# Kernel optimization log

Hardware: AMD Instinct MI355X
Metric: run time of the kernel (lower is better)

Reference implementation:

```python
import jax, jax.numpy as jnp
import numpy as np

B, N, H = 512, 128, 256      # graphs, nodes per graph, hidden
NH, HD = 8, 32               # heads, head dim
DEG = 8
E = B * N * DEG              # 524288 edges
BN_EPS = 1e-5


def setup_inputs() -> dict:
    key = jax.random.key(0)
    ks = jax.random.split(key, 16)

    def w(k, shape):
        return jax.random.normal(k, shape, dtype=jnp.float32) * 0.02

    # intra-graph random edges: base offset per graph, local src/dst in [0, N)
    base = jnp.repeat(jnp.arange(B, dtype=jnp.int32) * N, N * DEG)
    edge_src = base + jax.random.randint(ks[1], (E,), 0, N, dtype=jnp.int32)
    edge_dst = base + jax.random.randint(ks[2], (E,), 0, N, dtype=jnp.int32)

    return {
        "h": jax.random.normal(ks[0], (B * N, H), dtype=jnp.float32),
        "edge_src": edge_src,
        "edge_dst": edge_dst,
        "gin_w1": w(ks[3], (H, H)), "gin_b1": jnp.zeros((H,), jnp.float32),
        "gin_w2": w(ks[4], (H, H)), "gin_b2": jnp.zeros((H,), jnp.float32),
        "attn_in_w": w(ks[5], (3 * H, H)), "attn_in_b": jnp.zeros((3 * H,), jnp.float32),
        "attn_out_w": w(ks[6], (H, H)), "attn_out_b": jnp.zeros((H,), jnp.float32),
        "bn_local_g": jnp.ones((H,), jnp.float32), "bn_local_b": jnp.zeros((H,), jnp.float32),
        "bn_attn_g": jnp.ones((H,), jnp.float32), "bn_attn_b": jnp.zeros((H,), jnp.float32),
        "bn_out_g": jnp.ones((H,), jnp.float32), "bn_out_b": jnp.zeros((H,), jnp.float32),
        "ffn1_w": w(ks[7], (2 * H, H)), "ffn1_b": jnp.zeros((2 * H,), jnp.float32),
        "ffn2_w": w(ks[8], (H, 2 * H)), "ffn2_b": jnp.zeros((H,), jnp.float32),
    }


def _bn(x, g, b):
    # nn.BatchNorm1d training-mode forward: batch stats over node dim, biased var
    mean = jnp.mean(x, axis=0)
    var = jnp.mean(jnp.square(x - mean), axis=0)
    return g * (x - mean) * jax.lax.rsqrt(var + BN_EPS) + b


def _mha(x, in_w, in_b, out_w, out_b):
    # x: [B, N, H]; uniform graphs -> key_padding_mask is all-valid
    qkv = x @ in_w.T + in_b                           # [B, N, 3H]
    q, k, v = jnp.split(qkv, 3, axis=-1)
    def heads(t):
        return t.reshape(B, N, NH, HD).transpose(0, 2, 1, 3)  # [B, NH, N, HD]
    q, k, v = heads(q), heads(k), heads(v)
    scores = jnp.einsum('bhqd,bhkd->bhqk', q, k) / jnp.sqrt(jnp.float32(HD))
    att = jax.nn.softmax(scores, axis=-1)
    o = jnp.einsum('bhqk,bhkd->bhqd', att, v).transpose(0, 2, 1, 3).reshape(B, N, H)
    return o @ out_w.T + out_b


def reference(h, edge_src, edge_dst,
              gin_w1, gin_b1, gin_w2, gin_b2,
              attn_in_w, attn_in_b, attn_out_w, attn_out_b,
              bn_local_g, bn_local_b, bn_attn_g, bn_attn_b, bn_out_g, bn_out_b,
              ffn1_w, ffn1_b, ffn2_w, ffn2_b):
    # --- local GIN branch: (1+eps)*h + sum_{j in N(i)} h_j, eps=0, then 2-layer MLP
    agg = jax.ops.segment_sum(h[edge_src], edge_dst, num_segments=B * N)
    z = h + agg
    h_local = jax.nn.relu(z @ gin_w1.T + gin_b1) @ gin_w2.T + gin_b2
    h_local = _bn(h + h_local, bn_local_g, bn_local_b)

    # --- global attention branch (to_dense_batch is an exact reshape here)
    h_dense = h.reshape(B, N, H)
    h_attn = _mha(h_dense, attn_in_w, attn_in_b, attn_out_w, attn_out_b).reshape(B * N, H)
    h_attn = _bn(h + h_attn, bn_attn_g, bn_attn_b)

    # --- combine + FFN + out norm
    x = h_local + h_attn
    x = x + jax.nn.relu(x @ ffn1_w.T + ffn1_b) @ ffn2_w.T + ffn2_b
    return _bn(x, bn_out_g, bn_out_b)
```

## Files before the change

kernel.cpp:

```cpp
#include <hip/hip_runtime.h>
#include <hip/hip_bf16.h>

#define B_   512
#define N_   128
#define H_   256
#define NH_  8
#define HD_  32
#define DEG_ 8
#define R_   (B_ * N_)
#define E_   (B_ * N_ * DEG_)
#define EPG_ (N_ * DEG_)

typedef unsigned short u16;
typedef unsigned int u32;

typedef __attribute__((ext_vector_type(8))) short s16x8;
typedef __attribute__((ext_vector_type(4))) float f32x4;

__device__ __forceinline__ float b2f(u16 u) {
  union { u32 i; float f; } v;
  v.i = ((u32)u) << 16;
  return v.f;
}
__device__ __forceinline__ u16 f2b(float f) {
  union { float f; u32 u; } v;
  v.f = f;
  u32 r = (v.u + 0x7fffu + ((v.u >> 16) & 1u)) >> 16;
  return (u16)r;
}
__device__ __forceinline__ void ld4b(const u16* p, float* o) {
  ushort4 v = *(const ushort4*)p;
  o[0] = b2f(v.x); o[1] = b2f(v.y); o[2] = b2f(v.z); o[3] = b2f(v.w);
}

__device__ __forceinline__ int tix(int row, int col) {
  return ((row >> 7) << 15) + (((col >> 6) & 3) << 13) + ((row & 127) << 6) +
         (((((col >> 3) & 7) ^ (row & 7))) << 3) + (col & 7);
}


#define OFF_GW1 0
#define OFF_GB1 65536
#define OFF_GW2 65792
#define OFF_GB2 131328
#define OFF_AIW 131584
#define OFF_AIB 328192
#define OFF_AOW 328960
#define OFF_AOB 394496
#define OFF_F1W 394752
#define OFF_F1B 525824
#define OFF_F2W 526336
#define OFF_F2B 657408
#define W_TOTAL 657664

__global__ void zero_stats(float* __restrict__ st) {
  st[blockIdx.x * 256 + threadIdx.x] = 0.f;
}

__global__ __launch_bounds__(256) void cvt_h(const float* __restrict__ src,
                                             u16* __restrict__ dst) {
  const int e = (blockIdx.x * 256 + threadIdx.x) * 4;
  const float4 v = *(const float4*)(src + e);
  ushort4 o;
  o.x = f2b(v.x); o.y = f2b(v.y); o.z = f2b(v.z); o.w = f2b(v.w);
  *(ushort4*)(dst + tix(e >> 8, e & 255)) = o;
}

__global__ __launch_bounds__(256) void cvt_w(
    const float* s0, const float* s1, const float* s2, const float* s3,
    const float* s4, const float* s5, const float* s6, const float* s7,
    const float* s8, const float* s9, const float* s10, const float* s11,
    u16* __restrict__ dst) {
  const int sizes[12] = {65536, 256, 65536, 256, 196608, 768,
                         65536, 256, 131072, 512, 131072, 256};
  const float* srcs[12] = {s0, s1, s2, s3, s4, s5, s6, s7, s8, s9, s10, s11};
  int gid = (blockIdx.x * 256 + threadIdx.x) * 4;
  if (gid >= W_TOTAL) return;
  int seg = 0, off = gid;
  while (off >= sizes[seg]) { off -= sizes[seg]; seg++; }
  const float4 v = *(const float4*)(srcs[seg] + off);
  ushort4 o;
  o.x = f2b(v.x); o.y = f2b(v.y); o.z = f2b(v.z); o.w = f2b(v.w);
  *(ushort4*)(dst + gid) = o;
}

#define SROWS_ 32

__global__ __launch_bounds__(256) void agg_kernel(
    const u16* __restrict__ h, const int* __restrict__ esrc,
    const int* __restrict__ edst, u16* __restrict__ z) {
  __shared__ int s_src[EPG_];
  __shared__ int s_cnt[SROWS_];
  __shared__ int s_off[SROWS_ + 1];
  __shared__ int s_pos[SROWS_];
  const int g = blockIdx.x;
  const int r0 = blockIdx.y * SROWS_;
  const int t = threadIdx.x;

  if (t < SROWS_) s_cnt[t] = 0;
  __syncthreads();

  const int ebase = g * EPG_;
  int dl[4], sg[4];
#pragma unroll
  for (int i = 0; i < 4; i++) {
    const int e = ebase + t + i * 256;
    sg[i] = esrc[e];
    dl[i] = edst[e] - g * N_ - r0;
    if ((unsigned)dl[i] < SROWS_) atomicAdd(&s_cnt[dl[i]], 1);
  }
  __syncthreads();
  if (t == 0) {
    int acc = 0;
#pragma unroll
    for (int i = 0; i < SROWS_; i++) { s_off[i] = acc; acc += s_cnt[i]; }
    s_off[SROWS_] = acc;
  }
  __syncthreads();
  if (t < SROWS_) s_pos[t] = s_off[t];
  __syncthreads();
#pragma unroll
  for (int i = 0; i < 4; i++) {
    if ((unsigned)dl[i] < SROWS_) {
      const int slot = atomicAdd(&s_pos[dl[i]], 1);
      s_src[slot] = sg[i];
    }
  }
  __syncthreads();

  const int rg = t >> 5;
  const int c0 = (t & 31) * 8;
  for (int ib = 0; ib < SROWS_; ib += 8) {
    const int i = ib + rg;
    const int row = g * N_ + r0 + i;
    float acc[8];
    {
      const s16x8 v = *(const s16x8*)(h + tix(row, c0));
#pragma unroll
      for (int j = 0; j < 8; j++) acc[j] = b2f((u16)v[j]);
    }
    const int e0 = s_off[i], e1 = s_off[i + 1];
    for (int e = e0; e < e1; e++) {
      const int src = s_src[e];
      const s16x8 v = *(const s16x8*)(h + tix(src, c0));
#pragma unroll
      for (int j = 0; j < 8; j++) acc[j] += b2f((u16)v[j]);
    }
    s16x8 o;
#pragma unroll
    for (int j = 0; j < 8; j++) o[j] = (short)f2b(acc[j]);
    *(s16x8*)(z + tix(row, c0)) = o;
  }
}

template <int NC, int K, int RELU, int RES, int STATS, int ASPLIT, int CMODE>
__global__ __launch_bounds__(256) void gemm_mfma(
    const u16* A, const u16* A2,
    const u16* __restrict__ W, const u16* __restrict__ bias,
    const u16* res, u16* C0, u16* C1, u16* C2,
    float* __restrict__ gsum, float* __restrict__ gsq) {
  __shared__ u16 As[2][128 * 64] __attribute__((aligned(16)));
  __shared__ u16 Bs[2][128 * 64] __attribute__((aligned(16)));

  const int t = threadIdx.x;
  const int wave = t >> 6, lane = t & 63;
  const int wr = wave >> 1, wc = wave & 1;
  const int quad = lane >> 4, ln15 = lane & 15;
  const int row0 = blockIdx.x * 128, col0 = blockIdx.y * 128;

  f32x4 acc[4][4];
#pragma unroll
  for (int i = 0; i < 4; i++)
#pragma unroll
    for (int j = 0; j < 4; j++) acc[i][j] = (f32x4){0.f, 0.f, 0.f, 0.f};

  auto stage = [&](int b, int kt) {
    const u16* Ab;
    int ksl;
    if (ASPLIT) {
      if (kt < 256) { Ab = A; ksl = kt >> 6; } else { Ab = A2; ksl = (kt - 256) >> 6; }
    } else {
      Ab = A; ksl = kt >> 6;
    }
    const u16* abase = Ab + ((size_t)blockIdx.x << 15) + (ksl << 13);
#pragma unroll
    for (int i = 0; i < 4; i++) {
      const int fid = t + i * 256;
      __builtin_amdgcn_global_load_lds(
          (const __attribute__((address_space(1))) void*)(abase + fid * 8),
          (__attribute__((address_space(3))) void*)(&As[b][fid * 8]), 16, 0, 0);
      const int row = fid >> 3;
      const int segp = (fid & 7) ^ (row & 7);
      const u16* gw = W + (size_t)(col0 + row) * K + kt + segp * 8;
      __builtin_amdgcn_global_load_lds(
          (const __attribute__((address_space(1))) void*)gw,
          (__attribute__((address_space(3))) void*)(&Bs[b][fid * 8]), 16, 0, 0);
    }
  };

  stage(0, 0);
  for (int kt = 0; kt < K; kt += 64) {
    const int cur = (kt >> 6) & 1;
    if (kt + 64 < K) {
      stage(cur ^ 1, kt + 64);
      asm volatile("s_waitcnt vmcnt(8)" ::: "memory");
    } else {
      asm volatile("s_waitcnt vmcnt(0)" ::: "memory");
    }
    __builtin_amdgcn_s_barrier();
#pragma unroll
    for (int ks = 0; ks < 64; ks += 32) {
      s16x8 af[4], bf[4];
#pragma unroll
      for (int i = 0; i < 4; i++) {
        const int ra = wr * 64 + i * 16 + ln15;
        af[i] = *(const s16x8*)(
            &As[cur][ra * 64 + ((((ks >> 3) + quad) ^ (ra & 7)) * 8)]);
      }
#pragma unroll
      for (int j = 0; j < 4; j++) {
        const int rb = wc * 64 + j * 16 + ln15;
        bf[j] = *(const s16x8*)(
            &Bs[cur][rb * 64 + ((((ks >> 3) + quad) ^ (rb & 7)) * 8)]);
      }
#pragma unroll
      for (int i = 0; i < 4; i++)
#pragma unroll
        for (int j = 0; j < 4; j++)
          acc[i][j] = __builtin_amdgcn_mfma_f32_16x16x32_bf16(af[i], bf[j], acc[i][j], 0, 0, 0);
    }
    __builtin_amdgcn_s_barrier();
  }

  const int cbase = col0 + wc * 64;
  u16* Cb;
  int coff;
  if (CMODE) {
    const int chunk = col0 >> 8;
    Cb = (chunk == 0) ? C0 : ((chunk == 1) ? C1 : C2);
    coff = (col0 & 255) + wc * 64;
  } else {
    Cb = C0; coff = cbase;
  }

  float bs[4];
#pragma unroll
  for (int j = 0; j < 4; j++) bs[j] = b2f(bias[cbase + j * 16 + ln15]);

  float ssum[4] = {}, ssq[4] = {};
#pragma unroll
  for (int i = 0; i < 4; i++) {
    const int rbase = row0 + wr * 64 + i * 16 + quad * 4;
#pragma unroll
    for (int reg = 0; reg < 4; reg++) {
      const int row = rbase + reg;
#pragma unroll
      for (int j = 0; j < 4; j++) {
        float val = acc[i][j][reg] + bs[j];
        if (RELU) val = fmaxf(val, 0.f);
        if (RES) val += b2f(res[tix(row, cbase + j * 16 + ln15)]);
        Cb[tix(row, coff + j * 16 + ln15)] = f2b(val);
        if (STATS) { ssum[j] += val; ssq[j] += val * val; }
      }
    }
  }

  if (STATS) {
#pragma unroll
    for (int j = 0; j < 4; j++) {
      float s = ssum[j];
      s += __shfl_xor(s, 16);
      s += __shfl_xor(s, 32);
      float q = ssq[j];
      q += __shfl_xor(q, 16);
      q += __shfl_xor(q, 32);
      if (lane < 16) {
        atomicAdd(&gsum[cbase + j * 16 + lane], s);
        atomicAdd(&gsq[cbase + j * 16 + lane], q);
      }
    }
  }
}

__global__ __launch_bounds__(256) void attn_mfma(
    const u16* q, const u16* __restrict__ k,
    const u16* __restrict__ v, u16* o) {
  __shared__ u16 lds[21760] __attribute__((aligned(16)));
  u16* Vt = lds;
  u16* Qs = lds + 4352;
  u16* Ks = lds + 4352 + 5120;
  u16* P  = lds + 4352;

  const int g = blockIdx.x >> 3;
  const int hd = blockIdx.x & 7;
  const int t = threadIdx.x;
  const int wave = t >> 6, lane = t & 63;
  const int quad = lane >> 4, ln15 = lane & 15;
  const int strip = wave * 32;
  const float scale = 0.1767766952966369f;

#pragma unroll
  for (int i = 0; i < 4; i++) {
    const int fid = t + i * 256;
    const int row = fid >> 3;
    const int seg = fid & 7;
    const int gidx = tix(g * N_ + row, hd * HD_ + seg * 4);
    const ushort4 qv = *(const ushort4*)(q + gidx);
    const ushort4 kv = *(const ushort4*)(k + gidx);
    const ushort4 vv = *(const ushort4*)(v + gidx);
    ushort4 qs;
    qs.x = f2b(b2f(qv.x) * scale); qs.y = f2b(b2f(qv.y) * scale);
    qs.z = f2b(b2f(qv.z) * scale); qs.w = f2b(b2f(qv.w) * scale);
    *(ushort4*)(Qs + row * 40 + seg * 4) = qs;
    *(ushort4*)(Ks + row * 40 + seg * 4) = kv;
    Vt[(seg * 4 + 0) * 136 + row] = vv.x;
    Vt[(seg * 4 + 1) * 136 + row] = vv.y;
    Vt[(seg * 4 + 2) * 136 + row] = vv.z;
    Vt[(seg * 4 + 3) * 136 + row] = vv.w;
  }
  __syncthreads();

  s16x8 af[2], bf[8];
#pragma unroll
  for (int mi = 0; mi < 2; mi++)
    af[mi] = *(const s16x8*)(Qs + (strip + mi * 16 + ln15) * 40 + quad * 8);
#pragma unroll
  for (int nj = 0; nj < 8; nj++)
    bf[nj] = *(const s16x8*)(Ks + (nj * 16 + ln15) * 40 + quad * 8);

  f32x4 acc[2][8];
#pragma unroll
  for (int mi = 0; mi < 2; mi++)
#pragma unroll
    for (int nj = 0; nj < 8; nj++)
      acc[mi][nj] = __builtin_amdgcn_mfma_f32_16x16x32_bf16(
          af[mi], bf[nj], (f32x4){0.f, 0.f, 0.f, 0.f}, 0, 0, 0);

  __syncthreads();

#pragma unroll
  for (int mi = 0; mi < 2; mi++) {
#pragma unroll
    for (int reg = 0; reg < 4; reg++) {
      float mx = acc[mi][0][reg];
#pragma unroll
      for (int j = 1; j < 8; j++) mx = fmaxf(mx, acc[mi][j][reg]);
      mx = fmaxf(mx, __shfl_xor(mx, 1));
      mx = fmaxf(mx, __shfl_xor(mx, 2));
      mx = fmaxf(mx, __shfl_xor(mx, 4));
      mx = fmaxf(mx, __shfl_xor(mx, 8));
      float e[8], s = 0.f;
#pragma unroll
      for (int j = 0; j < 8; j++) { e[j] = __expf(acc[mi][j][reg] - mx); s += e[j]; }
      s += __shfl_xor(s, 1);
      s += __shfl_xor(s, 2);
      s += __shfl_xor(s, 4);
      s += __shfl_xor(s, 8);
      const float inv = 1.f / s;
      const int prow = strip + mi * 16 + quad * 4 + reg;
#pragma unroll
      for (int j = 0; j < 8; j++)
        P[prow * 136 + j * 16 + ln15] = f2b(e[j] * inv);
    }
  }
  __syncthreads();

  f32x4 acc2[2][2];
#pragma unroll
  for (int mi = 0; mi < 2; mi++)
#pragma unroll
    for (int nj = 0; nj < 2; nj++) acc2[mi][nj] = (f32x4){0.f, 0.f, 0.f, 0.f};
#pragma unroll
  for (int kt = 0; kt < 4; kt++) {
    s16x8 paf[2], vbf[2];
#pragma unroll
    for (int mi = 0; mi < 2; mi++)
      paf[mi] = *(const s16x8*)(P + (strip + mi * 16 + ln15) * 136 + kt * 32 + quad * 8);
#pragma unroll
    for (int nj = 0; nj < 2; nj++)
      vbf[nj] = *(const s16x8*)(Vt + (nj * 16 + ln15) * 136 + kt * 32 + quad * 8);
#pragma unroll
    for (int mi = 0; mi < 2; mi++)
#pragma unroll
      for (int nj = 0; nj < 2; nj++)
        acc2[mi][nj] = __builtin_amdgcn_mfma_f32_16x16x32_bf16(
            paf[mi], vbf[nj], acc2[mi][nj], 0, 0, 0);
  }

#pragma unroll
  for (int mi = 0; mi < 2; mi++)
#pragma unroll
    for (int nj = 0; nj < 2; nj++)
#pragma unroll
      for (int reg = 0; reg < 4; reg++) {
        const int row = strip + mi * 16 + quad * 4 + reg;
        o[tix(g * N_ + row, hd * HD_ + nj * 16 + ln15)] =
            f2b(acc2[mi][nj][reg]);
      }
}

__global__ void bn_finalize(const float* __restrict__ sum,
                            const float* __restrict__ sq,
                            const float* __restrict__ g,
                            const float* __restrict__ bb,
                            float* __restrict__ a, float* __restrict__ b) {
  const int c = threadIdx.x;
  const float mean = sum[c] * (1.f / R_);
  const float var = fmaxf(sq[c] * (1.f / R_) - mean * mean, 0.f);
  const float ai = g[c] * rsqrtf(var + 1e-5f);
  a[c] = ai;
  b[c] = bb[c] - mean * ai;
}

__global__ __launch_bounds__(256) void combine_kernel(
    const u16* __restrict__ rl, const u16* __restrict__ ra,
    const float* __restrict__ st, u16* __restrict__ x) {
  const int e = (blockIdx.x * 256 + threadIdx.x) * 4;
  const int col = e & 255;
  const int idx = tix(e >> 8, col);
  float rl4[4], ra4[4];
  ld4b(rl + idx, rl4);
  ld4b(ra + idx, ra4);
  const float* al = st + 1536;
  const float* bl = st + 1792;
  const float* aa = st + 2048;
  const float* ba = st + 2304;
  ushort4 o;
  u16* ov = (u16*)&o;
#pragma unroll
  for (int j = 0; j < 4; j++)
    ov[j] = f2b(al[col + j] * rl4[j] + bl[col + j] + aa[col + j] * ra4[j] + ba[col + j]);
  *(ushort4*)(x + idx) = o;
}

__global__ __launch_bounds__(256) void final_kernel(
    const u16* __restrict__ y, const float* __restrict__ st,
    float* __restrict__ out) {
  const int e = (blockIdx.x * 256 + threadIdx.x) * 4;
  const int col = e & 255;
  float y4[4];
  ld4b(y + tix(e >> 8, col), y4);
  const float* ao = st + 2560;
  const float* bo = st + 2816;
  float4 o;
  o.x = ao[col + 0] * y4[0] + bo[col + 0];
  o.y = ao[col + 1] * y4[1] + bo[col + 1];
  o.z = ao[col + 2] * y4[2] + bo[col + 2];
  o.w = ao[col + 3] * y4[3] + bo[col + 3];
  *(float4*)(out + e) = o;
}

extern "C" void kernel_launch(void* const* d_in, const int* in_sizes, int n_in,
                              void* d_out, int out_size, void* d_ws, size_t ws_size,
                              hipStream_t stream) {
  const float* h = (const float*)d_in[0];
  const int* esrc = (const int*)d_in[1];
  const int* edst = (const int*)d_in[2];
  const float* bn_local_g = (const float*)d_in[11];
  const float* bn_local_b = (const float*)d_in[12];
  const float* bn_attn_g = (const float*)d_in[13];
  const float* bn_attn_b = (const float*)d_in[14];
  const float* bn_out_g = (const float*)d_in[15];
  const float* bn_out_b = (const float*)d_in[16];

  const size_t RH = (size_t)R_ * H_;
  float* stats = (float*)d_ws;
  u16* WB = (u16*)((char*)d_ws + 65536);
  u16* Hb = (u16*)((char*)d_ws + 65536 + 2097152);
  u16* S1 = Hb + RH;
  u16* S2 = S1 + RH;
  u16* OD = (u16*)d_out;
  float* outf = (float*)d_out;

  zero_stats<<<12, 256, 0, stream>>>(stats);
  cvt_h<<<(int)(RH / 4 / 256), 256, 0, stream>>>(h, Hb);
  cvt_w<<<(W_TOTAL / 4 + 255) / 256, 256, 0, stream>>>(
      (const float*)d_in[3], (const float*)d_in[4], (const float*)d_in[5],
      (const float*)d_in[6], (const float*)d_in[7], (const float*)d_in[8],
      (const float*)d_in[9], (const float*)d_in[10], (const float*)d_in[17],
      (const float*)d_in[18], (const float*)d_in[19], (const float*)d_in[20], WB);

  gemm_mfma<768, 256, 0, 0, 0, 0, 1><<<dim3(512, 6), 256, 0, stream>>>(
      Hb, nullptr, WB + OFF_AIW, WB + OFF_AIB, nullptr, S1, S2, OD, nullptr, nullptr);
  attn_mfma<<<B_ * NH_, 256, 0, stream>>>(S1, S2, OD, S1);
  gemm_mfma<256, 256, 0, 1, 1, 0, 0><<<dim3(512, 2), 256, 0, stream>>>(
      S1, nullptr, WB + OFF_AOW, WB + OFF_AOB, Hb, S2, nullptr, nullptr,
      stats + 512, stats + 768);
  agg_kernel<<<dim3(B_, 4), 256, 0, stream>>>(Hb, esrc, edst, OD);
  gemm_mfma<256, 256, 1, 0, 0, 0, 0><<<dim3(512, 2), 256, 0, stream>>>(
      OD, nullptr, WB + OFF_GW1, WB + OFF_GB1, nullptr, S1, nullptr, nullptr,
      nullptr, nullptr);
  gemm_mfma<256, 256, 0, 1, 1, 0, 0><<<dim3(512, 2), 256, 0, stream>>>(
      S1, nullptr, WB + OFF_GW2, WB + OFF_GB2, Hb, OD, nullptr, nullptr,
      stats + 0, stats + 256);

  bn_finalize<<<1, 256, 0, stream>>>(stats + 0, stats + 256, bn_local_g,
                                     bn_local_b, stats + 1536, stats + 1792);
  bn_finalize<<<1, 256, 0, stream>>>(stats + 512, stats + 768, bn_attn_g,
                                     bn_attn_b, stats + 2048, stats + 2304);

  combine_kernel<<<(int)(RH / 4 / 256), 256, 0, stream>>>(OD, S2, stats, S1);
  gemm_mfma<512, 256, 1, 0, 0, 0, 1><<<dim3(512, 4), 256, 0, stream>>>(
      S1, nullptr, WB + OFF_F1W, WB + OFF_F1B, nullptr, S2, OD, nullptr,
      nullptr, nullptr);
  gemm_mfma<256, 512, 0, 1, 1, 1, 0><<<dim3(512, 2), 256, 0, stream>>>(
      S2, OD, WB + OFF_F2W, WB + OFF_F2B, S1, S1, nullptr, nullptr,
      stats + 1024, stats + 1280);

  bn_finalize<<<1, 256, 0, stream>>>(stats + 1024, stats + 1280, bn_out_g,
                                     bn_out_b, stats + 2560, stats + 2816);
  final_kernel<<<(int)(RH / 4 / 256), 256, 0, stream>>>(S1, stats, outf);
}
```

Measured before the change: 612.9 us.

## Fuse two-layer MLPs into one kernel keeping hidden activations in LDS

Adds a fused_mlp kernel that loads a 128-row input tile into LDS once, computes each 128-column chunk of the first GEMM with bias and ReLU into an LDS buffer, and immediately accumulates it into the second GEMM. The output is written with the residual added and BatchNorm statistics accumulated. It replaces the GIN MLP pair and the FFN pair of gemm_mfma launches, removing the intermediate activation round-trips through global memory and the A-split path. The trade-off is much larger LDS use and accumulator register pressure (launch bounds 256,2), and a second-layer weight load with no double buffering.

New measurement: 595.9 us. 1.03x faster.

```diff
diff --git a/kernel.cpp b/kernel.cpp
--- a/kernel.cpp
+++ b/kernel.cpp
@@ -36,6 +36,12 @@
 __device__ __forceinline__ int tix(int row, int col) {
   return ((row >> 7) << 15) + (((col >> 6) & 3) << 13) + ((row & 127) << 6) +
          (((((col >> 3) & 7) ^ (row & 7))) << 3) + (col & 7);
+}
+
+__device__ __forceinline__ void glds16(const u16* g, u16* l) {
+  __builtin_amdgcn_global_load_lds(
+      (const __attribute__((address_space(1))) void*)g,
+      (__attribute__((address_space(3))) void*)l, 16, 0, 0);
 }
 
 
@@ -153,9 +159,9 @@
   }
 }
 
-template <int NC, int K, int RELU, int RES, int STATS, int ASPLIT, int CMODE>
+template <int NC, int K, int RELU, int RES, int STATS, int CMODE>
 __global__ __launch_bounds__(256) void gemm_mfma(
-    const u16* A, const u16* A2,
+    const u16* A,
     const u16* __restrict__ W, const u16* __restrict__ bias,
     const u16* res, u16* C0, u16* C1, u16* C2,
     float* __restrict__ gsum, float* __restrict__ gsq) {
@@ -175,26 +181,14 @@
     for (int j = 0; j < 4; j++) acc[i][j] = (f32x4){0.f, 0.f, 0.f, 0.f};
 
   auto stage = [&](int b, int kt) {
-    const u16* Ab;
-    int ksl;
-    if (ASPLIT) {
-      if (kt < 256) { Ab = A; ksl = kt >> 6; } else { Ab = A2; ksl = (kt - 256) >> 6; }
-    } else {
-      Ab = A; ksl = kt >> 6;
-    }
-    const u16* abase = Ab + ((size_t)blockIdx.x << 15) + (ksl << 13);
+    const u16* abase = A + ((size_t)blockIdx.x << 15) + ((kt >> 6) << 13);
 #pragma unroll
     for (int i = 0; i < 4; i++) {
       const int fid = t + i * 256;
-      __builtin_amdgcn_global_load_lds(
-          (const __attribute__((address_space(1))) void*)(abase + fid * 8),
-          (__attribute__((address_space(3))) void*)(&As[b][fid * 8]), 16, 0, 0);
+      glds16(abase + fid * 8, &As[b][fid * 8]);
       const int row = fid >> 3;
       const int segp = (fid & 7) ^ (row & 7);
-      const u16* gw = W + (size_t)(col0 + row) * K + kt + segp * 8;
-      __builtin_amdgcn_global_load_lds(
-          (const __attribute__((address_space(1))) void*)gw,
-          (__attribute__((address_space(3))) void*)(&Bs[b][fid * 8]), 16, 0, 0);
+      glds16(W + (size_t)(col0 + row) * K + kt + segp * 8, &Bs[b][fid * 8]);
     }
   };
 
@@ -278,6 +272,193 @@
         atomicAdd(&gsum[cbase + j * 16 + lane], s);
         atomicAdd(&gsq[cbase + j * 16 + lane], q);
       }
+    }
+  }
+}
+
+template <int CHUNKS, int RES_LDS>
+__global__ __launch_bounds__(256, 2) void fused_mlp(
+    const u16* A, const u16* __restrict__ W1, const u16* __restrict__ b1,
+    const u16* __restrict__ W2, const u16* __restrict__ b2,
+    const u16* resg, u16* C,
+    float* __restrict__ gsum, float* __restrict__ gsq) {
+  __shared__ u16 xs[4 * 128 * 64] __attribute__((aligned(16)));
+  __shared__ u16 tc[128 * 128] __attribute__((aligned(16)));
+  __shared__ u16 Wst[2][128 * 64] __attribute__((aligned(16)));
+
+  const int t = threadIdx.x;
+  const int wave = t >> 6, lane = t & 63;
+  const int wr = wave >> 1, wc = wave & 1;
+  const int quad = lane >> 4, ln15 = lane & 15;
+  const int row0 = blockIdx.x * 128;
+  const int K2 = CHUNKS * 128;
+
+  {
+    const u16* abase = A + ((size_t)blockIdx.x << 15);
+#pragma unroll
+    for (int i = 0; i < 16; i++) {
+      const int fid = t + i * 256;
+      glds16(abase + fid * 8, xs + fid * 8);
+    }
+  }
+
+  f32x4 acc2[4][8];
+#pragma unroll
+  for (int i = 0; i < 4; i++)
+#pragma unroll
+    for (int j = 0; j < 8; j++) acc2[i][j] = (f32x4){0.f, 0.f, 0.f, 0.f};
+
+  auto tca = [&](int row, int col) {
+    const int s0 = col >> 3;
+    return row * 128 + (((s0 & 8) | ((s0 ^ row) & 7)) << 3) + (col & 7);
+  };
+
+  for (int c = 0; c < CHUNKS; c++) {
+    f32x4 acc1[4][4];
+#pragma unroll
+    for (int i = 0; i < 4; i++)
+#pragma unroll
+      for (int j = 0; j < 4; j++) acc1[i][j] = (f32x4){0.f, 0.f, 0.f, 0.f};
+
+    auto stage1 = [&](int b, int kt) {
+#pragma unroll
+      for (int i = 0; i < 4; i++) {
+        const int fid = t + i * 256;
+        const int row = fid >> 3;
+        const int segp = (fid & 7) ^ (row & 7);
+        glds16(W1 + (size_t)(c * 128 + row) * 256 + kt + segp * 8,
+               &Wst[b][fid * 8]);
+      }
+    };
+
+    stage1(0, 0);
+    for (int kt = 0; kt < 256; kt += 64) {
+      const int cur = (kt >> 6) & 1;
+      if (kt + 64 < 256) {
+        stage1(cur ^ 1, kt + 64);
+        asm volatile("s_waitcnt vmcnt(4)" ::: "memory");
+      } else {
+        asm volatile("s_waitcnt vmcnt(0)" ::: "memory");
+      }
+      __builtin_amdgcn_s_barrier();
+#pragma unroll
+      for (int ks = 0; ks < 64; ks += 32) {
+        s16x8 af[4], bf[4];
+#pragma unroll
+        for (int i = 0; i < 4; i++) {
+          const int ra = wr * 64 + i * 16 + ln15;
+          af[i] = *(const s16x8*)(
+              &xs[(kt >> 6) * 8192 + ra * 64 +
+                  ((((ks >> 3) + quad) ^ (ra & 7)) * 8)]);
+        }
+#pragma unroll
+        for (int j = 0; j < 4; j++) {
+          const int rb = wc * 64 + j * 16 + ln15;
+          bf[j] = *(const s16x8*)(
+              &Wst[cur][rb * 64 + ((((ks >> 3) + quad) ^ (rb & 7)) * 8)]);
+        }
+#pragma unroll
+        for (int i = 0; i < 4; i++)
+#pragma unroll
+          for (int j = 0; j < 4; j++)
+            acc1[i][j] = __builtin_amdgcn_mfma_f32_16x16x32_bf16(af[i], bf[j], acc1[i][j], 0, 0, 0);
+      }
+      __builtin_amdgcn_s_barrier();
+    }
+
+    {
+      float b1s[4];
+#pragma unroll
+      for (int j = 0; j < 4; j++)
+        b1s[j] = b2f(b1[c * 128 + wc * 64 + j * 16 + ln15]);
+#pragma unroll
+      for (int i = 0; i < 4; i++)
+#pragma unroll
+        for (int reg = 0; reg < 4; reg++) {
+          const int rowl = wr * 64 + i * 16 + quad * 4 + reg;
+#pragma unroll
+          for (int j = 0; j < 4; j++) {
+            const int coll = wc * 64 + j * 16 + ln15;
+            tc[tca(rowl, coll)] = f2b(fmaxf(acc1[i][j][reg] + b1s[j], 0.f));
+          }
+        }
+    }
+    __syncthreads();
+
+    for (int ks2 = 0; ks2 < 2; ks2++) {
+#pragma unroll
+      for (int i = 0; i < 8; i++) {
+        const int fid = t + i * 256;
+        const int row = fid >> 3;
+        const int segp = (fid & 7) ^ (row & 7);
+        glds16(W2 + (size_t)row * K2 + c * 128 + ks2 * 64 + segp * 8,
+               &Wst[0][fid * 8]);
+      }
+      asm volatile("s_waitcnt vmcnt(0)" ::: "memory");
+      __builtin_amdgcn_s_barrier();
+#pragma unroll
+      for (int ksl = 0; ksl < 64; ksl += 32) {
+        s16x8 af[4], bf[8];
+#pragma unroll
+        for (int i = 0; i < 4; i++) {
+          const int ra = wr * 64 + i * 16 + ln15;
+          af[i] = *(const s16x8*)(&tc[tca(ra, ks2 * 64 + ksl + quad * 8)]);
+        }
+#pragma unroll
+        for (int j = 0; j < 8; j++) {
+          const int rb = wc * 128 + j * 16 + ln15;
+          bf[j] = *(const s16x8*)(
+              &Wst[0][rb * 64 + ((((ksl >> 3) + quad) ^ (rb & 7)) * 8)]);
+        }
+#pragma unroll
+        for (int i = 0; i < 4; i++)
+#pragma unroll
+          for (int j = 0; j < 8; j++)
+            acc2[i][j] = __builtin_amdgcn_mfma_f32_16x16x32_bf16(af[i], bf[j], acc2[i][j], 0, 0, 0);
+      }
+      __builtin_amdgcn_s_barrier();
+    }
+  }
+
+  float bs2[8];
+#pragma unroll
+  for (int j = 0; j < 8; j++)
+    bs2[j] = b2f(b2[wc * 128 + j * 16 + ln15]);
+
+  float ssum[8] = {}, ssq[8] = {};
+#pragma unroll
+  for (int i = 0; i < 4; i++) {
+#pragma unroll
+    for (int reg = 0; reg < 4; reg++) {
+      const int rowl = wr * 64 + i * 16 + quad * 4 + reg;
+      const int row = row0 + rowl;
+#pragma unroll
+      for (int j = 0; j < 8; j++) {
+        const int col = wc * 128 + j * 16 + ln15;
+        float val = acc2[i][j][reg] + bs2[j];
+        if (RES_LDS) {
+          val += b2f(xs[(col >> 6) * 8192 + rowl * 64 +
+                        ((((col >> 3) & 7) ^ (rowl & 7)) << 3) + (col & 7)]);
+        } else {
+          val += b2f(resg[tix(row, col)]);
+        }
+        C[tix(row, col)] = f2b(val);
+        ssum[j] += val; ssq[j] += val * val;
+      }
+    }
+  }
+
+#pragma unroll
+  for (int j = 0; j < 8; j++) {
+    float s = ssum[j];
+    s += __shfl_xor(s, 16);
+    s += __shfl_xor(s, 32);
+    float q = ssq[j];
+    q += __shfl_xor(q, 16);
+    q += __shfl_xor(q, 32);
+    if (lane < 16) {
+      atomicAdd(&gsum[wc * 128 + j * 16 + lane], s);
+      atomicAdd(&gsq[wc * 128 + j * 16 + lane], q);
     }
   }
 }
@@ -480,18 +661,15 @@
       (const float*)d_in[9], (const float*)d_in[10], (const float*)d_in[17],
       (const float*)d_in[18], (const float*)d_in[19], (const float*)d_in[20], WB);
 
-  gemm_mfma<768, 256, 0, 0, 0, 0, 1><<<dim3(512, 6), 256, 0, stream>>>(
-      Hb, nullptr, WB + OFF_AIW, WB + OFF_AIB, nullptr, S1, S2, OD, nullptr, nullptr);
+  gemm_mfma<768, 256, 0, 0, 0, 1><<<dim3(512, 6), 256, 0, stream>>>(
+      Hb, WB + OFF_AIW, WB + OFF_AIB, nullptr, S1, S2, OD, nullptr, nullptr);
   attn_mfma<<<B_ * NH_, 256, 0, stream>>>(S1, S2, OD, S1);
-  gemm_mfma<256, 256, 0, 1, 1, 0, 0><<<dim3(512, 2), 256, 0, stream>>>(
-      S1, nullptr, WB + OFF_AOW, WB + OFF_AOB, Hb, S2, nullptr, nullptr,
+  gemm_mfma<256, 256, 0, 1, 1, 0><<<dim3(512, 2), 256, 0, stream>>>(
+      S1, WB + OFF_AOW, WB + OFF_AOB, Hb, S2, nullptr, nullptr,
       stats + 512, stats + 768);
   agg_kernel<<<dim3(B_, 4), 256, 0, stream>>>(Hb, esrc, edst, OD);
-  gemm_mfma<256, 256, 1, 0, 0, 0, 0><<<dim3(512, 2), 256, 0, stream>>>(
-      OD, nullptr, WB + OFF_GW1, WB + OFF_GB1, nullptr, S1, nullptr, nullptr,
-      nullptr, nullptr);
-  gemm_mfma<256, 256, 0, 1, 1, 0, 0><<<dim3(512, 2), 256, 0, stream>>>(
-      S1, nullptr, WB + OFF_GW2, WB + OFF_GB2, Hb, OD, nullptr, nullptr,
+  fused_mlp<2, 0><<<512, 256, 0, stream>>>(
+      OD, WB + OFF_GW1, WB + OFF_GB1, WB + OFF_GW2, WB + OFF_GB2, Hb, S1,
       stats + 0, stats + 256);
 
   bn_finalize<<<1, 256, 0, stream>>>(stats + 0, stats + 256, bn_local_g,
@@ -499,12 +677,9 @@
   bn_finalize<<<1, 256, 0, stream>>>(stats + 512, stats + 768, bn_attn_g,
                                      bn_attn_b, stats + 2048, stats + 2304);
 
-  combine_kernel<<<(int)(RH / 4 / 256), 256, 0, stream>>>(OD, S2, stats, S1);
-  gemm_mfma<512, 256, 1, 0, 0, 0, 1><<<dim3(512, 4), 256, 0, stream>>>(
-      S1, nullptr, WB + OFF_F1W, WB + OFF_F1B, nullptr, S2, OD, nullptr,
-      nullptr, nullptr);
-  gemm_mfma<256, 512, 0, 1, 1, 1, 0><<<dim3(512, 2), 256, 0, stream>>>(
-      S2, OD, WB + OFF_F2W, WB + OFF_F2B, S1, S1, nullptr, nullptr,
+  combine_kernel<<<(int)(RH / 4 / 256), 256, 0, stream>>>(S1, S2, stats, OD);
+  fused_mlp<4, 1><<<512, 256, 0, stream>>>(
+      OD, WB + OFF_F1W, WB + OFF_F1B, WB + OFF_F2W, WB + OFF_F2B, nullptr, S1,
       stats + 1024, stats + 1280);
 
   bn_finalize<<<1, 256, 0, stream>>>(stats + 1024, stats + 1280, bn_out_g,
```
